# Performance work log

Hardware: AMD Instinct MI355X
Metric: run time of the kernel (lower is better)

Reference implementation:

```python
import jax, jax.numpy as jnp
import numpy as np

B = 524288  # batch size
H = 4      # hidden dim


def _gru(x, h, Wih, Whh, bih, bhh):
    """PyTorch GRUCell semantics. x: [..., in], h: [..., H]."""
    gi = x @ Wih.T + bih          # [..., 3H]
    gh = h @ Whh.T + bhh          # [..., 3H]
    ir, iz, inn = jnp.split(gi, 3, axis=-1)
    hr, hz, hn = jnp.split(gh, 3, axis=-1)
    r = jax.nn.sigmoid(ir + hr)
    z = jax.nn.sigmoid(iz + hz)
    n = jnp.tanh(inn + r * hn)
    return (1.0 - z) * n + z * h


def setup_inputs() -> dict:
    key = jax.random.key(0)
    ks = jax.random.split(key, 16)
    s = 0.1
    return {
        "x": jax.random.normal(ks[0], (B, 18), dtype=jnp.float32),
        # fc_j_init: Linear(2, 4)
        "Wj": jax.random.normal(ks[1], (H, 2), dtype=jnp.float32) * s,
        "bj": jax.random.normal(ks[2], (H,), dtype=jnp.float32) * s,
        # fc_m_init: Linear(4, 4)
        "Wm": jax.random.normal(ks[3], (H, H), dtype=jnp.float32) * s,
        "bm": jax.random.normal(ks[4], (H,), dtype=jnp.float32) * s,
        # rnn_j: GRUCell(8, 4) (input is cat of two neighbor states)
        "Wih_j": jax.random.normal(ks[5], (3 * H, 2 * H), dtype=jnp.float32) * s,
        "Whh_j": jax.random.normal(ks[6], (3 * H, H), dtype=jnp.float32) * s,
        "bih_j": jax.random.normal(ks[7], (3 * H,), dtype=jnp.float32) * s,
        "bhh_j": jax.random.normal(ks[8], (3 * H,), dtype=jnp.float32) * s,
        # rnn_m: GRUCell(4, 4)
        "Wih_m": jax.random.normal(ks[9], (3 * H, H), dtype=jnp.float32) * s,
        "Whh_m": jax.random.normal(ks[10], (3 * H, H), dtype=jnp.float32) * s,
        "bih_m": jax.random.normal(ks[11], (3 * H,), dtype=jnp.float32) * s,
        "bhh_m": jax.random.normal(ks[12], (3 * H,), dtype=jnp.float32) * s,
        # fc_act: Linear(4, 1)
        "Wa": jax.random.normal(ks[13], (1, H), dtype=jnp.float32) * s,
        "ba": jax.random.normal(ks[14], (1,), dtype=jnp.float32) * s,
    }


def reference(x, Wj, bj, Wm, bm, Wih_j, Whh_j, bih_j, bhh_j,
              Wih_m, Whh_m, bih_m, bhh_m, Wa, ba):
    obs = x[:, :4]                       # [B, 4]
    j = x[:, 4:11]                       # [B, 7]
    jd = x[:, 11:18]                     # [B, 7]
    jcat = jnp.stack([j, jd], axis=-1)   # [B, 7, 2] per-joint (angle, vel)

    hj = jcat @ Wj.T + bj                # [B, 7, 4] joint hidden states
    hm = obs @ Wm.T + bm                 # [B, 4]   master hidden state

    zero_pad = jnp.zeros_like(hj[:, :1])  # [B, 1, 4] (node 6 has no right neighbor)
    for _ in range(7):
        hm_new = _gru(hj[:, 0], hm, Wih_m, Whh_m, bih_m, bhh_m)
        # left neighbor of node 0 is the master; of node i is node i-1
        left = jnp.concatenate([hm[:, None], hj[:, :6]], axis=1)   # [B, 7, 4]
        right = jnp.concatenate([hj[:, 1:], zero_pad], axis=1)     # [B, 7, 4]
        inp = jnp.concatenate([left, right], axis=-1)              # [B, 7, 8]
        hj = _gru(inp, hj, Wih_j, Whh_j, bih_j, bhh_j)             # all 7 nodes at once
        hm = hm_new

    acts = hj @ Wa.T + ba                # [B, 7, 1]
    return acts
```

## Files before the change

kernel.cpp:

```cpp
#include <hip/hip_runtime.h>


typedef _Float16 half2v __attribute__((ext_vector_type(2)));

__device__ __forceinline__ float fexp2(float x) { return __builtin_amdgcn_exp2f(x); }
__device__ __forceinline__ float frcp(float x)  { return __builtin_amdgcn_rcpf(x); }
__device__ __forceinline__ float fdot2(half2v a, half2v b, float c) {
    return __builtin_amdgcn_fdot2(a, b, c, false);
}
__device__ __forceinline__ half2v pkh(float a, float b) {
    return half2v{(_Float16)a, (_Float16)b};
}
__device__ __forceinline__ unsigned pku(float a, float b) {
    union { unsigned u; half2v h; } z; z.h = pkh(a, b); return z.u;
}
__device__ __forceinline__ half2v ldw(const unsigned* p, int i) {
    union { unsigned u; half2v h; } z; z.u = p[i]; return z.h;
}

__device__ __forceinline__ float gru_out(float pre_r, float pre_z,
                                         float inn, float hn, float h) {
    float er = fexp2(pre_r);
    float r  = frcp(1.0f + er);
    float ez = fexp2(pre_z);
    float narg = fmaf(r, hn, inn);
    float en = fexp2(narg);
    float t1 = ez + h;
    float t2 = h - ez;
    float num = fmaf(en, t1, t2);
    float s   = ez + 1.0f;
    float den = fmaf(en, s, s);
    return num * frcp(den);
}

#define U_PJRZ 0
#define U_PJNLR 48
#define U_PJNH 64
#define U_PMRZ 72
#define U_PMNI 104
#define U_PMNH 112
#define F_BRZJ 120
#define F_BINJ 128
#define F_BHNJ 132
#define F_BRZM 136
#define F_BINM 144
#define F_BHNM 148
#define F_WJ   152
#define F_BJ   160
#define F_WM   164
#define F_BM   180
#define F_WA   184
#define F_BA   188
#define W_TOT2 189

__global__ void pack_weights2(
    const float* __restrict__ Wj,    const float* __restrict__ bj,
    const float* __restrict__ Wm,    const float* __restrict__ bm,
    const float* __restrict__ Wih_j, const float* __restrict__ Whh_j,
    const float* __restrict__ bih_j, const float* __restrict__ bhh_j,
    const float* __restrict__ Wih_m, const float* __restrict__ Whh_m,
    const float* __restrict__ bih_m, const float* __restrict__ bhh_m,
    const float* __restrict__ Wa,    const float* __restrict__ ba,
    void* __restrict__ wsv)
{
    unsigned* wu = (unsigned*)wsv;
    float*    wf = (float*)wsv;
    int t = threadIdx.x;
    const float SN = -1.44269504088896f;
    const float ST =  2.88539008177793f;
    if (t < 48) {
        int g = t / 6, p = t % 6; float a, b;
        if (p < 4) { a = Wih_j[g*8 + 2*p];     b = Wih_j[g*8 + 2*p + 1]; }
        else       { a = Whh_j[g*4 + 2*(p-4)]; b = Whh_j[g*4 + 2*(p-4) + 1]; }
        wu[t] = pku(a * SN, b * SN);
    } else if (t < 64) {
        int i = t - 48, u = i / 4, p = i % 4;
        wu[t] = pku(Wih_j[(8+u)*8 + 2*p] * ST, Wih_j[(8+u)*8 + 2*p + 1] * ST);
    } else if (t < 72) {
        int i = t - 64, u = i / 2, p = i % 2;
        wu[t] = pku(Whh_j[(8+u)*4 + 2*p] * ST, Whh_j[(8+u)*4 + 2*p + 1] * ST);
    } else if (t < 104) {
        int i = t - 72, g = i / 4, p = i % 4; float a, b;
        if (p < 2) { a = Wih_m[g*4 + 2*p];     b = Wih_m[g*4 + 2*p + 1]; }
        else       { a = Whh_m[g*4 + 2*(p-2)]; b = Whh_m[g*4 + 2*(p-2) + 1]; }
        wu[t] = pku(a * SN, b * SN);
    } else if (t < 112) {
        int i = t - 104, u = i / 2, p = i % 2;
        wu[t] = pku(Wih_m[(8+u)*4 + 2*p] * ST, Wih_m[(8+u)*4 + 2*p + 1] * ST);
    } else if (t < 120) {
        int i = t - 112, u = i / 2, p = i % 2;
        wu[t] = pku(Whh_m[(8+u)*4 + 2*p] * ST, Whh_m[(8+u)*4 + 2*p + 1] * ST);
    } else if (t < 128) { wf[t] = (bih_j[t-120] + bhh_j[t-120]) * SN; }
    else if (t < 132)   { wf[t] = bih_j[8 + t - 128] * ST; }
    else if (t < 136)   { wf[t] = bhh_j[8 + t - 132] * ST; }
    else if (t < 144)   { wf[t] = (bih_m[t-136] + bhh_m[t-136]) * SN; }
    else if (t < 148)   { wf[t] = bih_m[8 + t - 144] * ST; }
    else if (t < 152)   { wf[t] = bhh_m[8 + t - 148] * ST; }
    else if (t < 160)   { wf[t] = Wj[t - 152]; }
    else if (t < 164)   { wf[t] = bj[t - 160]; }
    else if (t < 180)   { wf[t] = Wm[t - 164]; }
    else if (t < 184)   { wf[t] = bm[t - 180]; }
    else if (t < 188)   { wf[t] = Wa[t - 184]; }
    else if (t == 188)  { wf[t] = ba[0]; }
}

__global__ __launch_bounds__(256)
void aggreg_policy_dot2(
    const float* __restrict__ x, const void* __restrict__ wsv,
    float* __restrict__ out, int nrows)
{
    const unsigned* WU = (const unsigned*)wsv;
    const float*    WF = (const float*)wsv;
    int b = blockIdx.x * blockDim.x + threadIdx.x;
    if (b >= nrows) return;

    const float2* xr2 = (const float2*)(x + (long)b * 18);
    float xin[18];
    #pragma unroll
    for (int i = 0; i < 9; ++i) { float2 v = xr2[i]; xin[2*i] = v.x; xin[2*i+1] = v.y; }

    float hj[7][4], hm[4];
    half2v pj[7][2], pm[2];

    #pragma unroll
    for (int k = 0; k < 7; ++k) {
        #pragma unroll
        for (int u = 0; u < 4; ++u)
            hj[k][u] = fmaf(WF[F_WJ + u*2], xin[4 + k],
                       fmaf(WF[F_WJ + u*2 + 1], xin[11 + k], WF[F_BJ + u]));
        pj[k][0] = pkh(hj[k][0], hj[k][1]);
        pj[k][1] = pkh(hj[k][2], hj[k][3]);
    }
    #pragma unroll
    for (int u = 0; u < 4; ++u) {
        float a = WF[F_BM + u];
        #pragma unroll
        for (int v = 0; v < 4; ++v) a = fmaf(WF[F_WM + u*4 + v], xin[v], a);
        hm[u] = a;
    }
    pm[0] = pkh(hm[0], hm[1]);
    pm[1] = pkh(hm[2], hm[3]);

    #pragma unroll 1
    for (int it = 0; it < 7; ++it) {
        float hmn[4]; half2v pmn[2];
        {
            float pre[8], inn[4], hn[4];
            #pragma unroll
            for (int g = 0; g < 8; ++g) {
                float a = WF[F_BRZM + g];
                a = fdot2(pj[0][0], ldw(WU, U_PMRZ + g*4 + 0), a);
                a = fdot2(pj[0][1], ldw(WU, U_PMRZ + g*4 + 1), a);
                a = fdot2(pm[0],    ldw(WU, U_PMRZ + g*4 + 2), a);
                a = fdot2(pm[1],    ldw(WU, U_PMRZ + g*4 + 3), a);
                pre[g] = a;
            }
            #pragma unroll
            for (int u = 0; u < 4; ++u) {
                float a = WF[F_BINM + u];
                a = fdot2(pj[0][0], ldw(WU, U_PMNI + u*2 + 0), a);
                a = fdot2(pj[0][1], ldw(WU, U_PMNI + u*2 + 1), a);
                inn[u] = a;
                float c = WF[F_BHNM + u];
                c = fdot2(pm[0], ldw(WU, U_PMNH + u*2 + 0), c);
                c = fdot2(pm[1], ldw(WU, U_PMNH + u*2 + 1), c);
                hn[u] = c;
            }
            #pragma unroll
            for (int u = 0; u < 4; ++u)
                hmn[u] = gru_out(pre[u], pre[4 + u], inn[u], hn[u], hm[u]);
            pmn[0] = pkh(hmn[0], hmn[1]);
            pmn[1] = pkh(hmn[2], hmn[3]);
        }

        half2v opp[2];
        #pragma unroll
        for (int k = 0; k < 7; ++k) {
            half2v L0 = (k == 0) ? pm[0] : opp[0];
            half2v L1 = (k == 0) ? pm[1] : opp[1];
            half2v H0 = pj[k][0], H1 = pj[k][1];
            float pre[8], inn[4], hn[4];
            #pragma unroll
            for (int g = 0; g < 8; ++g) {
                float a = WF[F_BRZJ + g];
                a = fdot2(L0, ldw(WU, U_PJRZ + g*6 + 0), a);
                a = fdot2(L1, ldw(WU, U_PJRZ + g*6 + 1), a);
                if (k != 6) {
                    a = fdot2(pj[k+1][0], ldw(WU, U_PJRZ + g*6 + 2), a);
                    a = fdot2(pj[k+1][1], ldw(WU, U_PJRZ + g*6 + 3), a);
                }
                a = fdot2(H0, ldw(WU, U_PJRZ + g*6 + 4), a);
                a = fdot2(H1, ldw(WU, U_PJRZ + g*6 + 5), a);
                pre[g] = a;
            }
            #pragma unroll
            for (int u = 0; u < 4; ++u) {
                float a = WF[F_BINJ + u];
                a = fdot2(L0, ldw(WU, U_PJNLR + u*4 + 0), a);
                a = fdot2(L1, ldw(WU, U_PJNLR + u*4 + 1), a);
                if (k != 6) {
                    a = fdot2(pj[k+1][0], ldw(WU, U_PJNLR + u*4 + 2), a);
                    a = fdot2(pj[k+1][1], ldw(WU, U_PJNLR + u*4 + 3), a);
                }
                inn[u] = a;
                float c = WF[F_BHNJ + u];
                c = fdot2(H0, ldw(WU, U_PJNH + u*2 + 0), c);
                c = fdot2(H1, ldw(WU, U_PJNH + u*2 + 1), c);
                hn[u] = c;
            }
            float nh[4];
            #pragma unroll
            for (int u = 0; u < 4; ++u)
                nh[u] = gru_out(pre[u], pre[4 + u], inn[u], hn[u], hj[k][u]);
            opp[0] = pj[k][0]; opp[1] = pj[k][1];
            #pragma unroll
            for (int u = 0; u < 4; ++u) hj[k][u] = nh[u];
            pj[k][0] = pkh(nh[0], nh[1]);
            pj[k][1] = pkh(nh[2], nh[3]);
        }

        #pragma unroll
        for (int u = 0; u < 4; ++u) hm[u] = hmn[u];
        pm[0] = pmn[0]; pm[1] = pmn[1];
    }

    float* orow = out + (long)b * 7;
    #pragma unroll
    for (int k = 0; k < 7; ++k) {
        float a = WF[F_BA];
        #pragma unroll
        for (int u = 0; u < 4; ++u) a = fmaf(WF[F_WA + u], hj[k][u], a);
        orow[k] = a;
    }
}

__device__ __forceinline__ float sigmoid_f(float x) {
    return frcp(1.0f + fexp2(-1.44269504088896f * x));
}
__device__ __forceinline__ float tanh_f(float x) {
    float e = fexp2(2.88539008177793f * x);
    return 1.0f - 2.0f * frcp(1.0f + e);
}

__global__ __launch_bounds__(256) void aggreg_policy_fallback(
    const float* __restrict__ x,
    const float* __restrict__ Wj,    const float* __restrict__ bj,
    const float* __restrict__ Wm,    const float* __restrict__ bm,
    const float* __restrict__ Wih_j, const float* __restrict__ Whh_j,
    const float* __restrict__ bih_j, const float* __restrict__ bhh_j,
    const float* __restrict__ Wih_m, const float* __restrict__ Whh_m,
    const float* __restrict__ bih_m, const float* __restrict__ bhh_m,
    const float* __restrict__ Wa,    const float* __restrict__ ba,
    float* __restrict__ out, int nrows)
{
    int b = blockIdx.x * blockDim.x + threadIdx.x;
    if (b >= nrows) return;
    const float* xr = x + (long)b * 18;
    float obs[4], jv[7], jd[7];
    #pragma unroll
    for (int i = 0; i < 4; ++i) obs[i] = xr[i];
    #pragma unroll
    for (int i = 0; i < 7; ++i) jv[i] = xr[4 + i];
    #pragma unroll
    for (int i = 0; i < 7; ++i) jd[i] = xr[11 + i];
    float hj[7][4], hm[4];
    #pragma unroll
    for (int k = 0; k < 7; ++k)
        #pragma unroll
        for (int u = 0; u < 4; ++u)
            hj[k][u] = fmaf(Wj[u*2], jv[k], fmaf(Wj[u*2+1], jd[k], bj[u]));
    #pragma unroll
    for (int u = 0; u < 4; ++u) {
        float a = bm[u];
        #pragma unroll
        for (int v = 0; v < 4; ++v) a = fmaf(Wm[u*4+v], obs[v], a);
        hm[u] = a;
    }
    float bmrz[8], bjrz[8];
    #pragma unroll
    for (int g = 0; g < 8; ++g) { bmrz[g] = bih_m[g]+bhh_m[g]; bjrz[g] = bih_j[g]+bhh_j[g]; }
    #pragma unroll 1
    for (int it = 0; it < 7; ++it) {
        float hmn[4];
        {
            float pre[8], inn[4], hn[4];
            #pragma unroll
            for (int g = 0; g < 8; ++g) {
                float a = bmrz[g];
                #pragma unroll
                for (int v = 0; v < 4; ++v) a = fmaf(Wih_m[g*4+v], hj[0][v], a);
                #pragma unroll
                for (int v = 0; v < 4; ++v) a = fmaf(Whh_m[g*4+v], hm[v], a);
                pre[g] = a;
            }
            #pragma unroll
            for (int u = 0; u < 4; ++u) {
                float a = bih_m[8+u];
                #pragma unroll
                for (int v = 0; v < 4; ++v) a = fmaf(Wih_m[(8+u)*4+v], hj[0][v], a);
                inn[u] = a;
                float c = bhh_m[8+u];
                #pragma unroll
                for (int v = 0; v < 4; ++v) c = fmaf(Whh_m[(8+u)*4+v], hm[v], c);
                hn[u] = c;
            }
            #pragma unroll
            for (int u = 0; u < 4; ++u) {
                float r = sigmoid_f(pre[u]);
                float z = sigmoid_f(pre[4+u]);
                float n = tanh_f(fmaf(r, hn[u], inn[u]));
                hmn[u] = fmaf(z, hm[u]-n, n);
            }
        }
        float nh[7][4];
        #pragma unroll
        for (int k = 0; k < 7; ++k) {
            float L[4], R[4];
            #pragma unroll
            for (int u = 0; u < 4; ++u) {
                L[u] = (k == 0) ? hm[u] : hj[k-1][u];
                R[u] = (k == 6) ? 0.0f  : hj[k+1][u];
            }
            float pre[8], inn[4], hn[4];
            #pragma unroll
            for (int g = 0; g < 8; ++g) {
                float a = bjrz[g];
                #pragma unroll
                for (int v = 0; v < 4; ++v) a = fmaf(Wih_j[g*8+v], L[v], a);
                #pragma unroll
                for (int v = 0; v < 4; ++v) a = fmaf(Wih_j[g*8+4+v], R[v], a);
                #pragma unroll
                for (int v = 0; v < 4; ++v) a = fmaf(Whh_j[g*4+v], hj[k][v], a);
                pre[g] = a;
            }
            #pragma unroll
            for (int u = 0; u < 4; ++u) {
                float a = bih_j[8+u];
                #pragma unroll
                for (int v = 0; v < 4; ++v) a = fmaf(Wih_j[(8+u)*8+v], L[v], a);
                #pragma unroll
                for (int v = 0; v < 4; ++v) a = fmaf(Wih_j[(8+u)*8+4+v], R[v], a);
                inn[u] = a;
                float c = bhh_j[8+u];
                #pragma unroll
                for (int v = 0; v < 4; ++v) c = fmaf(Whh_j[(8+u)*4+v], hj[k][v], c);
                hn[u] = c;
            }
            #pragma unroll
            for (int u = 0; u < 4; ++u) {
                float r = sigmoid_f(pre[u]);
                float z = sigmoid_f(pre[4+u]);
                float n = tanh_f(fmaf(r, hn[u], inn[u]));
                nh[k][u] = fmaf(z, hj[k][u]-n, n);
            }
        }
        #pragma unroll
        for (int k = 0; k < 7; ++k)
            #pragma unroll
            for (int u = 0; u < 4; ++u) hj[k][u] = nh[k][u];
        #pragma unroll
        for (int u = 0; u < 4; ++u) hm[u] = hmn[u];
    }
    float* orow = out + (long)b * 7;
    #pragma unroll
    for (int k = 0; k < 7; ++k) {
        float a = ba[0];
        #pragma unroll
        for (int u = 0; u < 4; ++u) a = fmaf(Wa[u], hj[k][u], a);
        orow[k] = a;
    }
}

extern "C" void kernel_launch(void* const* d_in, const int* in_sizes, int n_in,
                              void* d_out, int out_size, void* d_ws, size_t ws_size,
                              hipStream_t stream) {
    const float* x     = (const float*)d_in[0];
    const float* Wj    = (const float*)d_in[1];
    const float* bj    = (const float*)d_in[2];
    const float* Wm    = (const float*)d_in[3];
    const float* bm    = (const float*)d_in[4];
    const float* Wih_j = (const float*)d_in[5];
    const float* Whh_j = (const float*)d_in[6];
    const float* bih_j = (const float*)d_in[7];
    const float* bhh_j = (const float*)d_in[8];
    const float* Wih_m = (const float*)d_in[9];
    const float* Whh_m = (const float*)d_in[10];
    const float* bih_m = (const float*)d_in[11];
    const float* bhh_m = (const float*)d_in[12];
    const float* Wa    = (const float*)d_in[13];
    const float* ba    = (const float*)d_in[14];
    float* out = (float*)d_out;

    int nrows = in_sizes[0] / 18;
    int block = 256;
    int grid = (nrows + block - 1) / block;

    if (ws_size >= W_TOT2 * sizeof(float)) {
        pack_weights2<<<1, 256, 0, stream>>>(
            Wj, bj, Wm, bm, Wih_j, Whh_j, bih_j, bhh_j,
            Wih_m, Whh_m, bih_m, bhh_m, Wa, ba, d_ws);
        aggreg_policy_dot2<<<grid, block, 0, stream>>>(x, d_ws, out, nrows);
    } else {
        aggreg_policy_fallback<<<grid, block, 0, stream>>>(
            x, Wj, bj, Wm, bm, Wih_j, Whh_j, bih_j, bhh_j,
            Wih_m, Whh_m, bih_m, bhh_m, Wa, ba, out, nrows);
    }
}
```

Measured before the change: 137.4 us.

## Drop fp32 hidden-state copies, keep only packed fp16 state, use cvt_pkrtz

The kernel no longer keeps a float copy of every hidden state next to the packed fp16 one. The GRU epilogue now rebuilds h from the packed half2 values, and the final projection uses fdot2 with packed Wa weights. Packing now uses the single cvt_pkrtz instruction. This is meant to cut register pressure (28+4 fewer live VGPRs) and conversion instructions, which could raise occupancy. In exchange the residual h term is rounded to fp16 (round-toward-zero) every step, which may reduce accuracy.

New measurement: 144.3 us. 5.0% more time.

```diff
diff --git a/kernel.cpp b/kernel.cpp
--- a/kernel.cpp
+++ b/kernel.cpp
@@ -9,28 +9,34 @@
     return __builtin_amdgcn_fdot2(a, b, c, false);
 }
 __device__ __forceinline__ half2v pkh(float a, float b) {
-    return half2v{(_Float16)a, (_Float16)b};
+    union { __fp16 __attribute__((ext_vector_type(2))) i; half2v o; } z;
+    z.i = __builtin_amdgcn_cvt_pkrtz(a, b);
+    return z.o;
 }
 __device__ __forceinline__ unsigned pku(float a, float b) {
-    union { unsigned u; half2v h; } z; z.h = pkh(a, b); return z.u;
+    union { unsigned u; half2v h; } z; z.h = half2v{(_Float16)a, (_Float16)b}; return z.u;
 }
 __device__ __forceinline__ half2v ldw(const unsigned* p, int i) {
     union { unsigned u; half2v h; } z; z.u = p[i]; return z.h;
 }
 
-__device__ __forceinline__ float gru_out(float pre_r, float pre_z,
-                                         float inn, float hn, float h) {
-    float er = fexp2(pre_r);
-    float r  = frcp(1.0f + er);
-    float ez = fexp2(pre_z);
-    float narg = fmaf(r, hn, inn);
-    float en = fexp2(narg);
-    float t1 = ez + h;
-    float t2 = h - ez;
-    float num = fmaf(en, t1, t2);
-    float s   = ez + 1.0f;
-    float den = fmaf(en, s, s);
-    return num * frcp(den);
+__device__ __forceinline__ void gru_ep(const float pre[8], const float inn[4],
+                                       const float hn[4], half2v hp0, half2v hp1,
+                                       float nh[4]) {
+    float h[4] = { (float)hp0[0], (float)hp0[1], (float)hp1[0], (float)hp1[1] };
+    #pragma unroll
+    for (int u = 0; u < 4; ++u) {
+        float er = fexp2(pre[u]);
+        float r  = frcp(1.0f + er);
+        float ez = fexp2(pre[4 + u]);
+        float en = fexp2(fmaf(r, hn[u], inn[u]));
+        float t1 = ez + h[u];
+        float t2 = h[u] - ez;
+        float num = fmaf(en, t1, t2);
+        float s   = ez + 1.0f;
+        float den = fmaf(en, s, s);
+        nh[u] = num * frcp(den);
+    }
 }
 
 #define U_PJRZ 0
@@ -39,19 +45,19 @@
 #define U_PMRZ 72
 #define U_PMNI 104
 #define U_PMNH 112
-#define F_BRZJ 120
-#define F_BINJ 128
-#define F_BHNJ 132
-#define F_BRZM 136
-#define F_BINM 144
-#define F_BHNM 148
-#define F_WJ   152
-#define F_BJ   160
-#define F_WM   164
-#define F_BM   180
-#define F_WA   184
-#define F_BA   188
-#define W_TOT2 189
+#define U_WA   120
+#define F_BRZJ 122
+#define F_BINJ 130
+#define F_BHNJ 134
+#define F_BRZM 138
+#define F_BINM 146
+#define F_BHNM 150
+#define F_WJ   154
+#define F_BJ   162
+#define F_WM   166
+#define F_BM   182
+#define F_BA   186
+#define W_TOT2 187
 
 __global__ void pack_weights2(
     const float* __restrict__ Wj,    const float* __restrict__ bj,
@@ -90,18 +96,18 @@
     } else if (t < 120) {
         int i = t - 112, u = i / 2, p = i % 2;
         wu[t] = pku(Whh_m[(8+u)*4 + 2*p] * ST, Whh_m[(8+u)*4 + 2*p + 1] * ST);
-    } else if (t < 128) { wf[t] = (bih_j[t-120] + bhh_j[t-120]) * SN; }
-    else if (t < 132)   { wf[t] = bih_j[8 + t - 128] * ST; }
-    else if (t < 136)   { wf[t] = bhh_j[8 + t - 132] * ST; }
-    else if (t < 144)   { wf[t] = (bih_m[t-136] + bhh_m[t-136]) * SN; }
-    else if (t < 148)   { wf[t] = bih_m[8 + t - 144] * ST; }
-    else if (t < 152)   { wf[t] = bhh_m[8 + t - 148] * ST; }
-    else if (t < 160)   { wf[t] = Wj[t - 152]; }
-    else if (t < 164)   { wf[t] = bj[t - 160]; }
-    else if (t < 180)   { wf[t] = Wm[t - 164]; }
-    else if (t < 184)   { wf[t] = bm[t - 180]; }
-    else if (t < 188)   { wf[t] = Wa[t - 184]; }
-    else if (t == 188)  { wf[t] = ba[0]; }
+    } else if (t < 122) { int i = t - 120; wu[t] = pku(Wa[2*i], Wa[2*i + 1]); }
+    else if (t < 130)   { wf[t] = (bih_j[t-122] + bhh_j[t-122]) * SN; }
+    else if (t < 134)   { wf[t] = bih_j[8 + t - 130] * ST; }
+    else if (t < 138)   { wf[t] = bhh_j[8 + t - 134] * ST; }
+    else if (t < 146)   { wf[t] = (bih_m[t-138] + bhh_m[t-138]) * SN; }
+    else if (t < 150)   { wf[t] = bih_m[8 + t - 146] * ST; }
+    else if (t < 154)   { wf[t] = bhh_m[8 + t - 150] * ST; }
+    else if (t < 162)   { wf[t] = Wj[t - 154]; }
+    else if (t < 166)   { wf[t] = bj[t - 162]; }
+    else if (t < 182)   { wf[t] = Wm[t - 166]; }
+    else if (t < 186)   { wf[t] = bm[t - 182]; }
+    else if (t == 186)  { wf[t] = ba[0]; }
 }
 
 __global__ __launch_bounds__(256)
@@ -119,31 +125,33 @@
     #pragma unroll
     for (int i = 0; i < 9; ++i) { float2 v = xr2[i]; xin[2*i] = v.x; xin[2*i+1] = v.y; }
 
-    float hj[7][4], hm[4];
     half2v pj[7][2], pm[2];
 
     #pragma unroll
     for (int k = 0; k < 7; ++k) {
-        #pragma unroll
-        for (int u = 0; u < 4; ++u)
-            hj[k][u] = fmaf(WF[F_WJ + u*2], xin[4 + k],
-                       fmaf(WF[F_WJ + u*2 + 1], xin[11 + k], WF[F_BJ + u]));
-        pj[k][0] = pkh(hj[k][0], hj[k][1]);
-        pj[k][1] = pkh(hj[k][2], hj[k][3]);
-    }
-    #pragma unroll
-    for (int u = 0; u < 4; ++u) {
-        float a = WF[F_BM + u];
-        #pragma unroll
-        for (int v = 0; v < 4; ++v) a = fmaf(WF[F_WM + u*4 + v], xin[v], a);
-        hm[u] = a;
-    }
-    pm[0] = pkh(hm[0], hm[1]);
-    pm[1] = pkh(hm[2], hm[3]);
+        float h0 = fmaf(WF[F_WJ + 0], xin[4 + k], fmaf(WF[F_WJ + 1], xin[11 + k], WF[F_BJ + 0]));
+        float h1 = fmaf(WF[F_WJ + 2], xin[4 + k], fmaf(WF[F_WJ + 3], xin[11 + k], WF[F_BJ + 1]));
+        float h2 = fmaf(WF[F_WJ + 4], xin[4 + k], fmaf(WF[F_WJ + 5], xin[11 + k], WF[F_BJ + 2]));
+        float h3 = fmaf(WF[F_WJ + 6], xin[4 + k], fmaf(WF[F_WJ + 7], xin[11 + k], WF[F_BJ + 3]));
+        pj[k][0] = pkh(h0, h1);
+        pj[k][1] = pkh(h2, h3);
+    }
+    {
+        float hm[4];
+        #pragma unroll
+        for (int u = 0; u < 4; ++u) {
+            float a = WF[F_BM + u];
+            #pragma unroll
+            for (int v = 0; v < 4; ++v) a = fmaf(WF[F_WM + u*4 + v], xin[v], a);
+            hm[u] = a;
+        }
+        pm[0] = pkh(hm[0], hm[1]);
+        pm[1] = pkh(hm[2], hm[3]);
+    }
 
     #pragma unroll 1
     for (int it = 0; it < 7; ++it) {
-        float hmn[4]; half2v pmn[2];
+        half2v pmn0, pmn1;
         {
             float pre[8], inn[4], hn[4];
             #pragma unroll
@@ -166,11 +174,10 @@
                 c = fdot2(pm[1], ldw(WU, U_PMNH + u*2 + 1), c);
                 hn[u] = c;
             }
-            #pragma unroll
-            for (int u = 0; u < 4; ++u)
-                hmn[u] = gru_out(pre[u], pre[4 + u], inn[u], hn[u], hm[u]);
-            pmn[0] = pkh(hmn[0], hmn[1]);
-            pmn[1] = pkh(hmn[2], hmn[3]);
+            float nh[4];
+            gru_ep(pre, inn, hn, pm[0], pm[1], nh);
+            pmn0 = pkh(nh[0], nh[1]);
+            pmn1 = pkh(nh[2], nh[3]);
         }
 
         half2v opp[2];
@@ -209,27 +216,22 @@
                 hn[u] = c;
             }
             float nh[4];
-            #pragma unroll
-            for (int u = 0; u < 4; ++u)
-                nh[u] = gru_out(pre[u], pre[4 + u], inn[u], hn[u], hj[k][u]);
-            opp[0] = pj[k][0]; opp[1] = pj[k][1];
-            #pragma unroll
-            for (int u = 0; u < 4; ++u) hj[k][u] = nh[u];
+            gru_ep(pre, inn, hn, H0, H1, nh);
+            opp[0] = H0; opp[1] = H1;
             pj[k][0] = pkh(nh[0], nh[1]);
             pj[k][1] = pkh(nh[2], nh[3]);
         }
 
-        #pragma unroll
-        for (int u = 0; u < 4; ++u) hm[u] = hmn[u];
-        pm[0] = pmn[0]; pm[1] = pmn[1];
+        pm[0] = pmn0; pm[1] = pmn1;
     }
 
     float* orow = out + (long)b * 7;
+    half2v wa0 = ldw(WU, U_WA + 0), wa1 = ldw(WU, U_WA + 1);
     #pragma unroll
     for (int k = 0; k < 7; ++k) {
         float a = WF[F_BA];
-        #pragma unroll
-        for (int u = 0; u < 4; ++u) a = fmaf(WF[F_WA + u], hj[k][u], a);
+        a = fdot2(pj[k][0], wa0, a);
+        a = fdot2(pj[k][1], wa1, a);
         orow[k] = a;
     }
 }
```
